# Kernel tuning notes

Hardware: AMD Instinct MI355X
Metric: run time of the kernel (lower is better)

The kernel has to match this reference:

```python
import jax, jax.numpy as jnp
import numpy as np

COEF = 0.1   # cfg.MODEL.SS.COEF
P, U, V, F = 8, 256, 256, 256 * 49  # pairs, u-proposals, v-proposals, ROI feat dim (256*7*7)


def setup_inputs() -> dict:
    key = jax.random.key(0)
    k1, k2 = jax.random.split(key)
    feat_u = jax.random.normal(k1, (P, U, F), dtype=jnp.float32)
    feat_v = jax.random.normal(k2, (P, V, F), dtype=jnp.float32)
    return {"feat_u": feat_u, "feat_v": feat_v}


def reference(feat_u, feat_v):
    # Pairwise squared L2 distance without materializing the O(U*V*F) expanded tensor:
    # ||u - v||^2 = ||u||^2 + ||v||^2 - 2 u.v
    uu = jnp.sum(feat_u * feat_u, axis=-1)                 # [P, U]
    vv = jnp.sum(feat_v * feat_v, axis=-1)                 # [P, V]
    uv = jnp.einsum('puf,pvf->puv', feat_u, feat_v)        # [P, U, V]
    dist = (uu[:, :, None] + vv[:, None, :] - 2.0 * uv) * COEF
    # Original applies softmax directly to the (positive) distances along v.
    score = jax.nn.softmax(dist, axis=-1)                  # [P, U, V]
    # neg_fea = score @ feat_v  (soft-kNN aggregation)
    neg_fea = jnp.einsum('puv,pvf->puf', score, feat_v)    # [P, U, F]
    pos_fea = feat_u.reshape(-1, F)                        # [P*U, F]
    # forward returns torch.cat([pos_fea, neg_fea], 0)
    return jnp.concatenate([pos_fea, neg_fea.reshape(-1, F)], axis=0)
```

## Files before the change

kernel.cpp:

```cpp
#include <hip/hip_runtime.h>
#include <cstdint>
#include <cstddef>

#define P_DIM 8
#define U_DIM 256
#define V_DIM 256
#define F_DIM 12544

typedef __attribute__((ext_vector_type(8))) short short8;
typedef __attribute__((ext_vector_type(8))) _Float16 half8;
typedef __attribute__((ext_vector_type(4))) float f32x4;

#define MFMA16B(a, b, c) __builtin_amdgcn_mfma_f32_16x16x32_bf16((a), (b), (c), 0, 0, 0)
#define MFMA16H(a, b, c) __builtin_amdgcn_mfma_f32_16x16x32_f16((a), (b), (c), 0, 0, 0)

#define GLOAD16(gsrc, ldsbase)                                                \
  __builtin_amdgcn_global_load_lds(                                           \
      (const __attribute__((address_space(1))) void*)(gsrc),                  \
      (__attribute__((address_space(3))) void*)(ldsbase), 16, 0, 0)

__device__ __forceinline__ unsigned short f2bf(float x) {
  unsigned u = __builtin_bit_cast(unsigned, x);
  u += 0x7FFFu + ((u >> 16) & 1u);
  return (unsigned short)(u >> 16);
}
__device__ __forceinline__ unsigned short f2h(float x) {
  return __builtin_bit_cast(unsigned short, (_Float16)x);
}

__global__ __launch_bounds__(256) void prep_fv(const float* __restrict__ fv,
                                               unsigned short* __restrict__ fvT,
                                               unsigned short* __restrict__ fvH,
                                               float* __restrict__ vvpart) {
  __shared__ unsigned short tile[64][65];
  __shared__ float vvp[64];
  int f0 = blockIdx.x * 64, v0 = blockIdx.y * 64, p = blockIdx.z;
  const float* src = fv + (size_t)p * V_DIM * F_DIM;
  unsigned short* dstH = fvH + (size_t)p * V_DIM * F_DIM;
  int t = threadIdx.x;
  #pragma unroll
  for (int i = 0; i < 4; ++i) {
    int g = t + i * 256;
    int r = g >> 4;
    int c4 = (g & 15) * 4;
    float4 x = *(const float4*)(src + (size_t)(v0 + r) * F_DIM + f0 + c4);
    tile[r][c4 + 0] = f2bf(x.x);
    tile[r][c4 + 1] = f2bf(x.y);
    tile[r][c4 + 2] = f2bf(x.z);
    tile[r][c4 + 3] = f2bf(x.w);
    ushort4 h;
    h.x = f2h(x.x); h.y = f2h(x.y); h.z = f2h(x.z); h.w = f2h(x.w);
    *(ushort4*)(dstH + (size_t)(v0 + r) * F_DIM + f0 + c4) = h;
    float ps = x.x * x.x + x.y * x.y + x.z * x.z + x.w * x.w;
    ps += __shfl_xor(ps, 1); ps += __shfl_xor(ps, 2);
    ps += __shfl_xor(ps, 4); ps += __shfl_xor(ps, 8);
    if ((t & 15) == 0) vvp[r] = ps;
  }
  __syncthreads();
  if (t < 64)
    vvpart[((size_t)blockIdx.x * P_DIM + p) * V_DIM + v0 + t] = vvp[t];
  unsigned short* dst = fvT + (size_t)p * F_DIM * V_DIM;
  #pragma unroll
  for (int i = 0; i < 2; ++i) {
    int g = t + i * 256;
    int f = g >> 3;
    int v8 = (g & 7) * 8;
    short8 o;
    #pragma unroll
    for (int j = 0; j < 8; ++j) o[j] = (short)tile[v8 + j][f];
    *(short8*)(dst + (size_t)(f0 + f) * V_DIM + v0 + v8) = o;
  }
}

__global__ __launch_bounds__(256) void vv_reduce(const float* __restrict__ vvpart,
                                                 float* __restrict__ vv) {
  int p = blockIdx.x >> 2;
  int vb = (blockIdx.x & 3) * 64;
  int vl = threadIdx.x & 63;
  int v = vb + vl;
  int js = threadIdx.x >> 6;
  float s = 0.f;
  for (int j = js; j < F_DIM / 64; j += 4)
    s += vvpart[((size_t)j * P_DIM + p) * V_DIM + v];
  __shared__ float red[4][64];
  red[js][vl] = s;
  __syncthreads();
  if (threadIdx.x < 64)
    vv[p * V_DIM + v] = red[0][vl] + red[1][vl] + red[2][vl] + red[3][vl];
}

__global__ __launch_bounds__(256) void copy_fu(const float4* __restrict__ src,
                                               float4* __restrict__ dst,
                                               ushort4* __restrict__ fuH, int n4) {
  for (int i = blockIdx.x * 256 + threadIdx.x; i < n4; i += gridDim.x * 256) {
    float4 x = src[i];
    dst[i] = x;
    ushort4 h;
    h.x = f2h(x.x); h.y = f2h(x.y); h.z = f2h(x.z); h.w = f2h(x.w);
    fuH[i] = h;
  }
}

__global__ __launch_bounds__(256, 2) void uv_gemm(const unsigned short* __restrict__ fuH,
                                                  const unsigned short* __restrict__ fvH,
                                                  float* __restrict__ part,
                                                  int splitk, int chunk) {
  int nwg = gridDim.x;
  int q = nwg >> 3, r = nwg & 7;
  int xcd = blockIdx.x & 7, ofs = blockIdx.x >> 3;
  int wgid = (xcd < r ? xcd * (q + 1) : r * (q + 1) + (xcd - r) * q) + ofs;
  int nt = wgid & 1, mt = (wgid >> 1) & 1, p = (wgid >> 2) & 7, ks = wgid >> 5;

  const unsigned short* A = fuH + ((size_t)p * U_DIM + mt * 128) * F_DIM;
  const unsigned short* B = fvH + ((size_t)p * V_DIM + nt * 128) * F_DIM;
  int k0 = ks * chunk;
  int nkt = chunk >> 6;

  __shared__ short AS[2][128 * 64], BS[2][128 * 64];

  int tid = threadIdx.x, lane = tid & 63, wid = tid >> 6;
  int wm = wid >> 1, wn = wid & 1;
  int rl = lane & 15;
  f32x4 acc[4][4] = {};
  short8 ra[4], rb[4];

#define LOADR(kg)                                                             \
  do {                                                                        \
    _Pragma("unroll") for (int j = 0; j < 4; ++j) {                           \
      int g = tid + j * 256;                                                  \
      int row = g >> 3, c = g & 7;                                            \
      ra[j] = *(const short8*)(A + (size_t)row * F_DIM + (kg) + c * 8);       \
      rb[j] = *(const short8*)(B + (size_t)row * F_DIM + (kg) + c * 8);       \
    }                                                                         \
  } while (0)

#define WRITES(buf)                                                           \
  do {                                                                        \
    _Pragma("unroll") for (int j = 0; j < 4; ++j) {                           \
      int g = tid + j * 256;                                                  \
      int row = g >> 3, c = g & 7;                                            \
      int off = (row * 128 + c * 16) ^ ((row & 7) << 4);                      \
      *(short8*)((char*)AS[buf] + off) = ra[j];                               \
      *(short8*)((char*)BS[buf] + off) = rb[j];                               \
    }                                                                         \
  } while (0)

  LOADR(k0);
  WRITES(0);
  __syncthreads();
  int cur = 0;
  for (int kt = 0; kt < nkt; ++kt) {
    bool more = (kt + 1 < nkt);
    if (more) LOADR(k0 + (kt + 1) * 64);
    const char* Ap = (const char*)AS[cur];
    const char* Bp = (const char*)BS[cur];
    #pragma unroll
    for (int kk = 0; kk < 2; ++kk) {
      int kbyte = kk * 64 + (lane >> 4) * 16;
      half8 ah[4], bh[4];
      #pragma unroll
      for (int m = 0; m < 4; ++m) {
        int row = wm * 64 + m * 16 + rl;
        int off = (row * 128 + kbyte) ^ ((row & 7) << 4);
        ah[m] = *(const half8*)(Ap + off);
      }
      #pragma unroll
      for (int n = 0; n < 4; ++n) {
        int row = wn * 64 + n * 16 + rl;
        int off = (row * 128 + kbyte) ^ ((row & 7) << 4);
        bh[n] = *(const half8*)(Bp + off);
      }
      #pragma unroll
      for (int m = 0; m < 4; ++m)
        #pragma unroll
        for (int n = 0; n < 4; ++n)
          acc[m][n] = MFMA16H(ah[m], bh[n], acc[m][n]);
    }
    if (more) WRITES(cur ^ 1);
    __syncthreads();
    cur ^= 1;
  }
#undef LOADR
#undef WRITES
  float* dst = part + ((size_t)ks * P_DIM + p) * U_DIM * V_DIM;
  int rq = lane >> 4;
  #pragma unroll
  for (int m = 0; m < 4; ++m)
    #pragma unroll
    for (int n = 0; n < 4; ++n)
      #pragma unroll
      for (int i = 0; i < 4; ++i) {
        int u = mt * 128 + wm * 64 + m * 16 + rq * 4 + i;
        int v = nt * 128 + wn * 64 + n * 16 + rl;
        dst[(size_t)u * V_DIM + v] = acc[m][n][i];
      }
}

__global__ __launch_bounds__(256) void reduce_softmax(const float* __restrict__ part,
                                                      const float* __restrict__ vv,
                                                      unsigned short* __restrict__ score,
                                                      int splitk) {
  int u = blockIdx.x & 255, p = blockIdx.x >> 8;
  int v = threadIdx.x;
  size_t base = ((size_t)p * U_DIM + u) * V_DIM + v;
  float s = 0.f;
  for (int k = 0; k < splitk; ++k)
    s += part[(size_t)k * (P_DIM * U_DIM * V_DIM) + base];
  float logit = 0.1f * vv[p * V_DIM + v] - 0.2f * s;
  float m = logit;
  #pragma unroll
  for (int off = 32; off >= 1; off >>= 1) m = fmaxf(m, __shfl_xor(m, off));
  __shared__ float red[4], red2[4];
  int lane = v & 63, wid = v >> 6;
  if (lane == 0) red[wid] = m;
  __syncthreads();
  m = fmaxf(fmaxf(red[0], red[1]), fmaxf(red[2], red[3]));
  float e = __expf(logit - m);
  float tsum = e;
  #pragma unroll
  for (int off = 32; off >= 1; off >>= 1) tsum += __shfl_xor(tsum, off);
  if (lane == 0) red2[wid] = tsum;
  __syncthreads();
  tsum = red2[0] + red2[1] + red2[2] + red2[3];
  score[base] = f2bf(e / tsum);
}

__global__ __launch_bounds__(256, 2) void pv_gemm(const unsigned short* __restrict__ score,
                                                  const unsigned short* __restrict__ fvT,
                                                  float* __restrict__ outneg) {
  int my = blockIdx.x;
  int bx = blockIdx.y;
  int p = blockIdx.z;
  int n0 = bx * 64;
  const unsigned short* Sc = score + ((size_t)p * U_DIM + my * 128) * V_DIM;
  const unsigned short* Bt = fvT + ((size_t)p * F_DIM + n0) * V_DIM;
  __shared__ short Bs[64 * 256];
  char* Bsp = (char*)Bs;
  int tid = threadIdx.x, lane = tid & 63, wid = tid >> 6;
  int rl = lane & 15, rq = lane >> 4;

  #pragma unroll
  for (int j = 0; j < 8; ++j) {
    int g = tid + j * 256;
    int row = g >> 5;
    int c = g & 31;
    int sc = c ^ (row & 7);
    int ldsbase = (wid * 64 + j * 256) * 16;
    GLOAD16(Bt + (size_t)row * V_DIM + sc * 8, Bsp + ldsbase);
  }

  short8 a[2][8];
  #pragma unroll
  for (int m = 0; m < 2; ++m)
    #pragma unroll
    for (int k = 0; k < 8; ++k)
      a[m][k] = *(const short8*)(Sc + (size_t)(wid * 32 + m * 16 + rl) * V_DIM
                                 + k * 32 + rq * 8);
  __syncthreads();

  f32x4 acc[2][4] = {};
  #pragma unroll
  for (int k = 0; k < 8; ++k) {
    #pragma unroll
    for (int n = 0; n < 4; ++n) {
      int row = n * 16 + rl;
      short8 b = *(const short8*)(Bsp + row * 512
                                  + ((k * 64 + rq * 16) ^ ((row & 7) << 4)));
      acc[0][n] = MFMA16B(a[0][k], b, acc[0][n]);
      acc[1][n] = MFMA16B(a[1][k], b, acc[1][n]);
    }
  }

  float* dst = outneg + ((size_t)p * U_DIM + my * 128) * F_DIM;
  #pragma unroll
  for (int m = 0; m < 2; ++m)
    #pragma unroll
    for (int n = 0; n < 4; ++n)
      #pragma unroll
      for (int i = 0; i < 4; ++i) {
        int u = wid * 32 + m * 16 + rq * 4 + i;
        int f = n0 + n * 16 + rl;
        dst[(size_t)u * F_DIM + f] = acc[m][n][i];
      }
}

extern "C" void kernel_launch(void* const* d_in, const int* in_sizes, int n_in,
                              void* d_out, int out_size, void* d_ws, size_t ws_size,
                              hipStream_t stream) {
  const float* fu = (const float*)d_in[0];
  const float* fv = (const float*)d_in[1];
  float* out = (float*)d_out;
  char* ws = (char*)d_ws;

  const size_t HVF = (size_t)P_DIM * F_DIM * V_DIM * 2;
  float* vv = (float*)ws;
  unsigned short* score = (unsigned short*)(ws + 8192);
  unsigned short* fvT = (unsigned short*)(ws + 8192 + 1048576);
  unsigned short* fuH = (unsigned short*)(ws + 8192 + 1048576 + HVF);
  unsigned short* fvH = (unsigned short*)(ws + 8192 + 1048576 + 2 * HVF);
  size_t vvpartBase = 8192 + 1048576 + 3 * HVF;
  float* vvpart = (float*)(ws + vvpartBase);
  size_t partBase = vvpartBase + (size_t)(F_DIM / 64) * P_DIM * V_DIM * 4;
  float* part = (float*)(ws + partBase);

  const size_t puv4 = (size_t)P_DIM * U_DIM * V_DIM * 4;
  int splitk = 1;
  const int cands[5] = {14, 7, 4, 2, 1};
  for (int i = 0; i < 5; ++i) {
    if (partBase + (size_t)cands[i] * puv4 <= ws_size) { splitk = cands[i]; break; }
  }
  int chunk = F_DIM / splitk;

  prep_fv<<<dim3(F_DIM / 64, V_DIM / 64, P_DIM), 256, 0, stream>>>(fv, fvT, fvH,
                                                                   vvpart);
  vv_reduce<<<P_DIM * 4, 256, 0, stream>>>(vvpart, vv);
  int n4 = (P_DIM * U_DIM * F_DIM) / 4;
  copy_fu<<<2048, 256, 0, stream>>>((const float4*)fu, (float4*)out,
                                    (ushort4*)fuH, n4);
  uv_gemm<<<splitk * 32, 256, 0, stream>>>(fuH, fvH, part, splitk, chunk);
  reduce_softmax<<<P_DIM * U_DIM, 256, 0, stream>>>(part, vv, score, splitk);
  pv_gemm<<<dim3(2, F_DIM / 64, P_DIM), 256, 0, stream>>>(
      score, fvT, out + (size_t)P_DIM * U_DIM * F_DIM);
}
```

Before: 196.2 us.

## Fuse fp16 conversion into uv_gemm loads, drop fp16 staging copies of inputs

The uv_gemm kernel now reads the fp32 inputs directly and converts them to fp16 while writing its shared-memory tiles. This removes the separate fp16 copies of feat_u and feat_v that were previously written to the workspace and read back. The split-K candidate list also gains 28, so more workgroups run when the workspace allows. In exchange the GEMM loads twice as many bytes per tile, holds more staging registers and does the conversion inline, which may lower occupancy or overlap.

```diff
diff --git a/kernel.cpp b/kernel.cpp
--- a/kernel.cpp
+++ b/kernel.cpp
@@ -24,19 +24,26 @@
   u += 0x7FFFu + ((u >> 16) & 1u);
   return (unsigned short)(u >> 16);
 }
-__device__ __forceinline__ unsigned short f2h(float x) {
-  return __builtin_bit_cast(unsigned short, (_Float16)x);
+
+__device__ __forceinline__ uint4 cvt8h(float4 a, float4 b) {
+  float x[8] = {a.x, a.y, a.z, a.w, b.x, b.y, b.z, b.w};
+  unsigned w[4];
+  #pragma unroll
+  for (int i = 0; i < 4; ++i) {
+    unsigned short lo = __builtin_bit_cast(unsigned short, (_Float16)x[2 * i]);
+    unsigned short hi = __builtin_bit_cast(unsigned short, (_Float16)x[2 * i + 1]);
+    w[i] = (unsigned)lo | ((unsigned)hi << 16);
+  }
+  return uint4{w[0], w[1], w[2], w[3]};
 }
 
 __global__ __launch_bounds__(256) void prep_fv(const float* __restrict__ fv,
                                                unsigned short* __restrict__ fvT,
-                                               unsigned short* __restrict__ fvH,
                                                float* __restrict__ vvpart) {
   __shared__ unsigned short tile[64][65];
   __shared__ float vvp[64];
   int f0 = blockIdx.x * 64, v0 = blockIdx.y * 64, p = blockIdx.z;
   const float* src = fv + (size_t)p * V_DIM * F_DIM;
-  unsigned short* dstH = fvH + (size_t)p * V_DIM * F_DIM;
   int t = threadIdx.x;
   #pragma unroll
   for (int i = 0; i < 4; ++i) {
@@ -48,9 +55,6 @@
     tile[r][c4 + 1] = f2bf(x.y);
     tile[r][c4 + 2] = f2bf(x.z);
     tile[r][c4 + 3] = f2bf(x.w);
-    ushort4 h;
-    h.x = f2h(x.x); h.y = f2h(x.y); h.z = f2h(x.z); h.w = f2h(x.w);
-    *(ushort4*)(dstH + (size_t)(v0 + r) * F_DIM + f0 + c4) = h;
     float ps = x.x * x.x + x.y * x.y + x.z * x.z + x.w * x.w;
     ps += __shfl_xor(ps, 1); ps += __shfl_xor(ps, 2);
     ps += __shfl_xor(ps, 4); ps += __shfl_xor(ps, 8);
@@ -89,20 +93,14 @@
     vv[p * V_DIM + v] = red[0][vl] + red[1][vl] + red[2][vl] + red[3][vl];
 }
 
-__global__ __launch_bounds__(256) void copy_fu(const float4* __restrict__ src,
-                                               float4* __restrict__ dst,
-                                               ushort4* __restrict__ fuH, int n4) {
-  for (int i = blockIdx.x * 256 + threadIdx.x; i < n4; i += gridDim.x * 256) {
-    float4 x = src[i];
-    dst[i] = x;
-    ushort4 h;
-    h.x = f2h(x.x); h.y = f2h(x.y); h.z = f2h(x.z); h.w = f2h(x.w);
-    fuH[i] = h;
-  }
-}
-
-__global__ __launch_bounds__(256, 2) void uv_gemm(const unsigned short* __restrict__ fuH,
-                                                  const unsigned short* __restrict__ fvH,
+__global__ __launch_bounds__(256) void copy_kernel(const float4* __restrict__ src,
+                                                   float4* __restrict__ dst, int n4) {
+  for (int i = blockIdx.x * 256 + threadIdx.x; i < n4; i += gridDim.x * 256)
+    dst[i] = src[i];
+}
+
+__global__ __launch_bounds__(256, 2) void uv_gemm(const float* __restrict__ fu,
+                                                  const float* __restrict__ fv,
                                                   float* __restrict__ part,
                                                   int splitk, int chunk) {
   int nwg = gridDim.x;
@@ -111,8 +109,8 @@
   int wgid = (xcd < r ? xcd * (q + 1) : r * (q + 1) + (xcd - r) * q) + ofs;
   int nt = wgid & 1, mt = (wgid >> 1) & 1, p = (wgid >> 2) & 7, ks = wgid >> 5;
 
-  const unsigned short* A = fuH + ((size_t)p * U_DIM + mt * 128) * F_DIM;
-  const unsigned short* B = fvH + ((size_t)p * V_DIM + nt * 128) * F_DIM;
+  const float* A = fu + ((size_t)p * U_DIM + mt * 128) * F_DIM;
+  const float* B = fv + ((size_t)p * V_DIM + nt * 128) * F_DIM;
   int k0 = ks * chunk;
   int nkt = chunk >> 6;
 
@@ -122,31 +120,33 @@
   int wm = wid >> 1, wn = wid & 1;
   int rl = lane & 15;
   f32x4 acc[4][4] = {};
-  short8 ra[4], rb[4];
+  float4 ra[8], rb[8];
 
 #define LOADR(kg)                                                             \
   do {                                                                        \
     _Pragma("unroll") for (int j = 0; j < 4; ++j) {                           \
       int g = tid + j * 256;                                                  \
       int row = g >> 3, c = g & 7;                                            \
-      ra[j] = *(const short8*)(A + (size_t)row * F_DIM + (kg) + c * 8);       \
-      rb[j] = *(const short8*)(B + (size_t)row * F_DIM + (kg) + c * 8);       \
+      const float* sa = A + (size_t)row * F_DIM + (kg) + c * 8;               \
+      ra[2 * j] = *(const float4*)sa; ra[2 * j + 1] = *(const float4*)(sa + 4);\
+      const float* sb = B + (size_t)row * F_DIM + (kg) + c * 8;               \
+      rb[2 * j] = *(const float4*)sb; rb[2 * j + 1] = *(const float4*)(sb + 4);\
     }                                                                         \
   } while (0)
 
-#define WRITES(buf)                                                           \
+#define CVTWRITE(buf)                                                         \
   do {                                                                        \
     _Pragma("unroll") for (int j = 0; j < 4; ++j) {                           \
       int g = tid + j * 256;                                                  \
       int row = g >> 3, c = g & 7;                                            \
       int off = (row * 128 + c * 16) ^ ((row & 7) << 4);                      \
-      *(short8*)((char*)AS[buf] + off) = ra[j];                               \
-      *(short8*)((char*)BS[buf] + off) = rb[j];                               \
+      *(uint4*)((char*)AS[buf] + off) = cvt8h(ra[2 * j], ra[2 * j + 1]);      \
+      *(uint4*)((char*)BS[buf] + off) = cvt8h(rb[2 * j], rb[2 * j + 1]);      \
     }                                                                         \
   } while (0)
 
   LOADR(k0);
-  WRITES(0);
+  CVTWRITE(0);
   __syncthreads();
   int cur = 0;
   for (int kt = 0; kt < nkt; ++kt) {
@@ -176,12 +176,12 @@
         for (int n = 0; n < 4; ++n)
           acc[m][n] = MFMA16H(ah[m], bh[n], acc[m][n]);
     }
-    if (more) WRITES(cur ^ 1);
+    if (more) CVTWRITE(cur ^ 1);
     __syncthreads();
     cur ^= 1;
   }
 #undef LOADR
-#undef WRITES
+#undef CVTWRITE
   float* dst = part + ((size_t)ks * P_DIM + p) * U_DIM * V_DIM;
   int rq = lane >> 4;
   #pragma unroll
@@ -296,28 +296,24 @@
   float* vv = (float*)ws;
   unsigned short* score = (unsigned short*)(ws + 8192);
   unsigned short* fvT = (unsigned short*)(ws + 8192 + 1048576);
-  unsigned short* fuH = (unsigned short*)(ws + 8192 + 1048576 + HVF);
-  unsigned short* fvH = (unsigned short*)(ws + 8192 + 1048576 + 2 * HVF);
-  size_t vvpartBase = 8192 + 1048576 + 3 * HVF;
+  size_t vvpartBase = 8192 + 1048576 + HVF;
   float* vvpart = (float*)(ws + vvpartBase);
   size_t partBase = vvpartBase + (size_t)(F_DIM / 64) * P_DIM * V_DIM * 4;
   float* part = (float*)(ws + partBase);
 
   const size_t puv4 = (size_t)P_DIM * U_DIM * V_DIM * 4;
   int splitk = 1;
-  const int cands[5] = {14, 7, 4, 2, 1};
-  for (int i = 0; i < 5; ++i) {
+  const int cands[6] = {28, 14, 7, 4, 2, 1};
+  for (int i = 0; i < 6; ++i) {
     if (partBase + (size_t)cands[i] * puv4 <= ws_size) { splitk = cands[i]; break; }
   }
   int chunk = F_DIM / splitk;
 
-  prep_fv<<<dim3(F_DIM / 64, V_DIM / 64, P_DIM), 256, 0, stream>>>(fv, fvT, fvH,
-                                                                   vvpart);
+  prep_fv<<<dim3(F_DIM / 64, V_DIM / 64, P_DIM), 256, 0, stream>>>(fv, fvT, vvpart);
   vv_reduce<<<P_DIM * 4, 256, 0, stream>>>(vvpart, vv);
   int n4 = (P_DIM * U_DIM * F_DIM) / 4;
-  copy_fu<<<2048, 256, 0, stream>>>((const float4*)fu, (float4*)out,
-                                    (ushort4*)fuH, n4);
-  uv_gemm<<<splitk * 32, 256, 0, stream>>>(fuH, fvH, part, splitk, chunk);
+  copy_kernel<<<2048, 256, 0, stream>>>((const float4*)fu, (float4*)out, n4);
+  uv_gemm<<<splitk * 32, 256, 0, stream>>>(fu, fv, part, splitk, chunk);
   reduce_softmax<<<P_DIM * U_DIM, 256, 0, stream>>>(part, vv, score, splitk);
   pv_gemm<<<dim3(2, F_DIM / 64, P_DIM), 256, 0, stream>>>(
       score, fvT, out + (size_t)P_DIM * U_DIM * F_DIM);
```

Result: slower. 225.9 us (+15.1%).

## Cover all 256 u rows per pv_gemm block and swap operands for vector stores

Applied to the files above, without the earlier changes.

Each pv_gemm block now covers all 256 u rows for a 64-column slice of F instead of 128 rows. Each fvT tile is therefore loaded into LDS once rather than twice, and the grid is halved. MFMA operands are swapped so the fv tile is the A operand and the scores the B operand. The accumulator layout then lets each lane write four contiguous floats as a vector store instead of scalar strided stores. Score fragments are double-buffered in registers across k steps, and the accumulator grows to 16 tiles, which raises register pressure and may cut occupancy.

```diff
diff --git a/kernel.cpp b/kernel.cpp
--- a/kernel.cpp
+++ b/kernel.cpp
@@ -228,11 +228,10 @@
 __global__ __launch_bounds__(256, 2) void pv_gemm(const unsigned short* __restrict__ score,
                                                   const unsigned short* __restrict__ fvT,
                                                   float* __restrict__ outneg) {
-  int my = blockIdx.x;
-  int bx = blockIdx.y;
-  int p = blockIdx.z;
+  int bx = blockIdx.x;
+  int p = blockIdx.y;
   int n0 = bx * 64;
-  const unsigned short* Sc = score + ((size_t)p * U_DIM + my * 128) * V_DIM;
+  const unsigned short* Sc = score + (size_t)p * U_DIM * V_DIM;
   const unsigned short* Bt = fvT + ((size_t)p * F_DIM + n0) * V_DIM;
   __shared__ short Bs[64 * 256];
   char* Bsp = (char*)Bs;
@@ -249,39 +248,53 @@
     GLOAD16(Bt + (size_t)row * V_DIM + sc * 8, Bsp + ldsbase);
   }
 
-  short8 a[2][8];
-  #pragma unroll
-  for (int m = 0; m < 2; ++m)
-    #pragma unroll
-    for (int k = 0; k < 8; ++k)
-      a[m][k] = *(const short8*)(Sc + (size_t)(wid * 32 + m * 16 + rl) * V_DIM
-                                 + k * 32 + rq * 8);
-  __syncthreads();
-
-  f32x4 acc[2][4] = {};
+  const unsigned short* ScW = Sc + (size_t)(wid * 64) * V_DIM;
+  short8 sc0[4], sc1[4];
+  #pragma unroll
+  for (int nu = 0; nu < 4; ++nu)
+    sc0[nu] = *(const short8*)(ScW + (size_t)(nu * 16 + rl) * V_DIM + rq * 8);
+  __syncthreads();
+
+  f32x4 acc[4][4] = {};
   #pragma unroll
   for (int k = 0; k < 8; ++k) {
-    #pragma unroll
-    for (int n = 0; n < 4; ++n) {
-      int row = n * 16 + rl;
-      short8 b = *(const short8*)(Bsp + row * 512
-                                  + ((k * 64 + rq * 16) ^ ((row & 7) << 4)));
-      acc[0][n] = MFMA16B(a[0][k], b, acc[0][n]);
-      acc[1][n] = MFMA16B(a[1][k], b, acc[1][n]);
+    if (k + 1 < 8) {
+      if ((k & 1) == 0) {
+        #pragma unroll
+        for (int nu = 0; nu < 4; ++nu)
+          sc1[nu] = *(const short8*)(ScW + (size_t)(nu * 16 + rl) * V_DIM
+                                     + (k + 1) * 32 + rq * 8);
+      } else {
+        #pragma unroll
+        for (int nu = 0; nu < 4; ++nu)
+          sc0[nu] = *(const short8*)(ScW + (size_t)(nu * 16 + rl) * V_DIM
+                                     + (k + 1) * 32 + rq * 8);
+      }
     }
-  }
-
-  float* dst = outneg + ((size_t)p * U_DIM + my * 128) * F_DIM;
-  #pragma unroll
-  for (int m = 0; m < 2; ++m)
-    #pragma unroll
-    for (int n = 0; n < 4; ++n)
-      #pragma unroll
-      for (int i = 0; i < 4; ++i) {
-        int u = wid * 32 + m * 16 + rq * 4 + i;
-        int f = n0 + n * 16 + rl;
-        dst[(size_t)u * F_DIM + f] = acc[m][n][i];
-      }
+    short8 fvf[4];
+    #pragma unroll
+    for (int mf = 0; mf < 4; ++mf) {
+      int row = mf * 16 + rl;
+      fvf[mf] = *(const short8*)(Bsp + row * 512
+                                 + ((k * 64 + rq * 16) ^ ((row & 7) << 4)));
+    }
+    #pragma unroll
+    for (int mf = 0; mf < 4; ++mf)
+      #pragma unroll
+      for (int nu = 0; nu < 4; ++nu)
+        acc[mf][nu] = MFMA16B(fvf[mf], ((k & 1) == 0 ? sc0 : sc1)[nu],
+                              acc[mf][nu]);
+  }
+
+  float* dst = outneg + (size_t)p * U_DIM * F_DIM;
+  #pragma unroll
+  for (int mf = 0; mf < 4; ++mf)
+    #pragma unroll
+    for (int nu = 0; nu < 4; ++nu) {
+      int u = wid * 64 + nu * 16 + rl;
+      int f = n0 + mf * 16 + rq * 4;
+      *(f32x4*)(dst + (size_t)u * F_DIM + f) = acc[mf][nu];
+    }
 }
 
 extern "C" void kernel_launch(void* const* d_in, const int* in_sizes, int n_in,
@@ -319,6 +332,6 @@
                                     (ushort4*)fuH, n4);
   uv_gemm<<<splitk * 32, 256, 0, stream>>>(fuH, fvH, part, splitk, chunk);
   reduce_softmax<<<P_DIM * U_DIM, 256, 0, stream>>>(part, vv, score, splitk);
-  pv_gemm<<<dim3(2, F_DIM / 64, P_DIM), 256, 0, stream>>>(
+  pv_gemm<<<dim3(F_DIM / 64, P_DIM), 256, 0, stream>>>(
       score, fvT, out + (size_t)P_DIM * U_DIM * F_DIM);
 }
```

After: 207.0 us. 5.5% more time.
